# Performance work log

Measured on AMD Instinct MI355X. Metric: run time of the kernel, lower is better.

The kernel has to match this reference:

```python
import jax, jax.numpy as jnp
import numpy as np

D_MODEL = 1024
NUM_HEADS = 16
HEAD_DIM = D_MODEL // NUM_HEADS


def setup_inputs() -> dict:
    key = jax.random.key(0)
    ks = jax.random.split(key, 5)
    x = jax.random.normal(ks[0], (2, 2048, D_MODEL), dtype=jnp.float32)
    # torch nn.Linear init scale ~ U(-1/sqrt(in), 1/sqrt(in)); use small normals
    s = 1.0 / np.sqrt(D_MODEL)
    W_qkv = jax.random.normal(ks[1], (D_MODEL, 3 * D_MODEL), dtype=jnp.float32) * s
    b_qkv = jax.random.normal(ks[2], (3 * D_MODEL,), dtype=jnp.float32) * s
    W_out = jax.random.normal(ks[3], (D_MODEL, D_MODEL), dtype=jnp.float32) * s
    b_out = jax.random.normal(ks[4], (D_MODEL,), dtype=jnp.float32) * s
    return {"x": x, "W_qkv": W_qkv, "b_qkv": b_qkv, "W_out": W_out, "b_out": b_out}


def reference(x, W_qkv, b_qkv, W_out, b_out):
    B, S, _ = x.shape
    qkv = x @ W_qkv + b_qkv                                  # [B,S,3D]
    qkv = qkv.reshape(B, S, NUM_HEADS, 3 * HEAD_DIM).transpose(0, 2, 1, 3)  # [B,H,S,3d]
    q, k, v = jnp.split(qkv, 3, axis=-1)                     # each [B,H,S,d]
    scale = 1.0 / np.sqrt(HEAD_DIM)
    scores = jnp.einsum("bhqd,bhkd->bhqk", q, k) * scale      # [B,H,S,S]
    attn = jax.nn.softmax(scores, axis=-1)
    values = jnp.einsum("bhqk,bhkd->bhqd", attn, v)           # [B,H,S,d]
    values = values.transpose(0, 2, 1, 3).reshape(B, S, D_MODEL)
    return values @ W_out + b_out
```

## Files before the change

### kernel.cpp

```cpp
#include <hip/hip_runtime.h>


#define D_MODEL 1024
#define NHEAD   16
#define HDIM    64
#define SEQ     2048
#define BATCH   2
#define NTOK    (BATCH * SEQ)

typedef float    f32x4  __attribute__((ext_vector_type(4)));
typedef float    f32x16 __attribute__((ext_vector_type(16)));
typedef _Float16 f16x8  __attribute__((ext_vector_type(8)));
typedef _Float16 f16x4  __attribute__((ext_vector_type(4)));

#define GLOBAL_LOAD_LDS16(gptr, lptr)                                            \
    __builtin_amdgcn_global_load_lds(                                            \
        (const __attribute__((address_space(1))) unsigned int*)(gptr),           \
        (__attribute__((address_space(3))) unsigned int*)(lptr), 16, 0, 0)

__global__ __launch_bounds__(256) void prep_kernel(
    const float* __restrict__ x, _Float16* __restrict__ xh,
    const float* __restrict__ Wqkv, _Float16* __restrict__ wq_t,
    const float* __restrict__ Wout, _Float16* __restrict__ wo_t)
{
    const int bx = blockIdx.x;
    const int tid = threadIdx.x;
    if (bx < 4096) {
        const int i = (bx * 256 + tid) * 4;
        const float4 v = *(const float4*)&x[i];
        f16x4 hh;
        hh[0] = (_Float16)v.x; hh[1] = (_Float16)v.y;
        hh[2] = (_Float16)v.z; hh[3] = (_Float16)v.w;
        *(f16x4*)&xh[i] = hh;
        return;
    }
    __shared__ float ts[64][65];
    const float* W; _Float16* Wt; int N, n0, k0;
    if (bx < 4096 + 768) {
        const int local = bx - 4096;
        W = Wqkv; Wt = wq_t; N = 3072;
        n0 = (local % 48) * 64; k0 = (local / 48) * 64;
    } else {
        const int local = bx - 4864;
        W = Wout; Wt = wo_t; N = 1024;
        n0 = (local % 16) * 64; k0 = (local / 16) * 64;
    }
    {
        const int r = tid >> 2, c = (tid & 3) << 4;
        const float* src = W + (size_t)(k0 + r) * N + n0 + c;
        #pragma unroll
        for (int u = 0; u < 4; ++u)
            *(float4*)&ts[r][c + u * 4] = *(const float4*)&src[u * 4];
    }
    __syncthreads();
    {
        const int n = tid >> 2, kg = (tid & 3) << 4;
        f16x8 v0, v1;
        #pragma unroll
        for (int j = 0; j < 8; ++j) {
            v0[j] = (_Float16)ts[kg + j][n];
            v1[j] = (_Float16)ts[kg + 8 + j][n];
        }
        _Float16* dst = Wt + (size_t)(n0 + n) * D_MODEL + k0 + kg;
        *(f16x8*)&dst[0] = v0;
        *(f16x8*)&dst[8] = v1;
    }
}

__global__ __launch_bounds__(512) void gemm_qkv_kernel(
    const _Float16* __restrict__ A, const _Float16* __restrict__ Bt,
    const float* __restrict__ bias, _Float16* __restrict__ Qh,
    _Float16* __restrict__ Ksw, _Float16* __restrict__ Vsw,
    int M, int N, int K)
{
    __shared__ _Float16 lds[3][2][4096];
    const int tid = threadIdx.x;
    const int wave = tid >> 6, lane = tid & 63;
    const int quad = lane >> 4, l16 = lane & 15;
    const int m0 = blockIdx.y * 128, n0 = blockIdx.x * 128;
    const int wr = wave >> 1, wc = wave & 1;

    f32x4 acc[2][4] = {};

    const bool isA = wave < 4;
    const _Float16* gsrc = isA ? (A + (size_t)m0 * K) : (Bt + (size_t)n0 * K);
    const int plane = isA ? 0 : 1;
    const int sbase = (wave & 3) * 2;

#define G1_STAGE(tt, bi) {                                                     \
        const int _k1 = (tt) * 32;                                             \
        _Pragma("unroll")                                                      \
        for (int _j = 0; _j < 2; ++_j) {                                       \
            const int _seg = sbase + _j;                                       \
            const int _row = ((_seg & 1) << 6) | lane;                         \
            GLOBAL_LOAD_LDS16(gsrc + (size_t)_row * K + _k1 + (_seg >> 1) * 8, \
                              &lds[bi][plane][_seg * 512]);                    \
        } }

#define G1_COMPUTE(bi) {                                                       \
        f16x8 a[2], b[4];                                                      \
        _Pragma("unroll")                                                      \
        for (int mt = 0; mt < 2; ++mt)                                         \
            a[mt] = *(const f16x8*)&lds[bi][0][quad * 1024 + (wr * 32 + mt * 16 + l16) * 8]; \
        _Pragma("unroll")                                                      \
        for (int nt = 0; nt < 4; ++nt)                                         \
            b[nt] = *(const f16x8*)&lds[bi][1][quad * 1024 + (wc * 64 + nt * 16 + l16) * 8]; \
        __builtin_amdgcn_s_setprio(1);                                         \
        _Pragma("unroll")                                                      \
        for (int mt = 0; mt < 2; ++mt)                                         \
            _Pragma("unroll")                                                  \
            for (int nt = 0; nt < 4; ++nt)                                     \
                acc[mt][nt] = __builtin_amdgcn_mfma_f32_16x16x32_f16(a[mt], b[nt], acc[mt][nt], 0, 0, 0); \
        __builtin_amdgcn_s_setprio(0); }

#define G1_KSTEP(t, gatestr) {                                                 \
        const int _cur = (t) % 3;                                              \
        if ((t) + 2 < nk) { G1_STAGE((t) + 2, ((t) + 2) % 3); }                \
        asm volatile("s_waitcnt " gatestr ::: "memory");                       \
        __builtin_amdgcn_s_barrier();                                          \
        __builtin_amdgcn_sched_barrier(0);                                     \
        G1_COMPUTE(_cur);                                                      \
        __builtin_amdgcn_sched_barrier(0);                                     \
        __builtin_amdgcn_s_barrier();                                          \
        __builtin_amdgcn_sched_barrier(0);                                     \
    }

    const int nk = K / 32;
    G1_STAGE(0, 0);
    G1_STAGE(1, 1);

    for (int t = 0; t < nk - 2; ++t)
        G1_KSTEP(t, "vmcnt(4)");
    G1_KSTEP(nk - 2, "vmcnt(2)");
    G1_KSTEP(nk - 1, "vmcnt(0)");

#undef G1_KSTEP
#undef G1_COMPUTE
#undef G1_STAGE

    const int colb = n0 + wc * 64;
    const int kind = (colb >> 6) % 3;
    const int h    = colb / 192;
    const int bb   = m0 >> 11;
    const int m0r  = m0 & 2047;
    const size_t hsz = (size_t)8 * SEQ * 8;

    if (kind == 0) {
        _Float16* qh = Qh + (size_t)m0 * D_MODEL + h * HDIM;
        #pragma unroll
        for (int nt = 0; nt < 4; ++nt) {
            const float bv = bias[colb + nt * 16 + l16];
            #pragma unroll
            for (int mt = 0; mt < 2; ++mt) {
                #pragma unroll
                for (int r = 0; r < 4; ++r) {
                    const int row = wr * 32 + mt * 16 + quad * 4 + r;
                    qh[(size_t)row * D_MODEL + nt * 16 + l16] = (_Float16)(acc[mt][nt][r] + bv);
                }
            }
        }
    } else if (kind == 1) {
        _Float16* kh = Ksw + (size_t)(bb * NHEAD + h) * hsz;
        #pragma unroll
        for (int nt = 0; nt < 4; ++nt) {
            const int d = nt * 16 + l16;
            const float bv = bias[colb + nt * 16 + l16];
            _Float16* kd = kh + (size_t)(d >> 3) * (SEQ * 8) + (d & 7);
            #pragma unroll
            for (int mt = 0; mt < 2; ++mt) {
                #pragma unroll
                for (int r = 0; r < 4; ++r) {
                    const int s = m0r + wr * 32 + mt * 16 + quad * 4 + r;
                    kd[(size_t)s * 8] = (_Float16)(acc[mt][nt][r] + bv);
                }
            }
        }
    } else {
        _Float16* vh = Vsw + (size_t)(bb * NHEAD + h) * hsz;
        #pragma unroll
        for (int nt = 0; nt < 4; ++nt) {
            const int d = nt * 16 + l16;
            const float bv = bias[colb + nt * 16 + l16];
            #pragma unroll
            for (int mt = 0; mt < 2; ++mt) {
                const int s0 = m0r + wr * 32 + mt * 16 + quad * 4;
                f16x4 pk;
                #pragma unroll
                for (int r = 0; r < 4; ++r)
                    pk[r] = (_Float16)(acc[mt][nt][r] + bv);
                *(f16x4*)&vh[(size_t)(s0 >> 3) * 512 + d * 8 + (s0 & 7)] = pk;
            }
        }
    }
}

__global__ __launch_bounds__(512) void gemm_out_kernel(
    const _Float16* __restrict__ A, const _Float16* __restrict__ Bt,
    const float* __restrict__ bias, float* __restrict__ Cout)
{
    const int K = D_MODEL, N = D_MODEL;
    __shared__ _Float16 ldsA[2][4096];
    __shared__ _Float16 ldsB[2][2048];
    const int tid = threadIdx.x;
    const int wave = tid >> 6, lane = tid & 63;
    const int quad = lane >> 4, l16 = lane & 15;
    const int m0 = blockIdx.y * 128, n0 = blockIdx.x * 64;
    const int wr = wave >> 1, wc = wave & 1;

    f32x4 acc[2][2] = {};

    if (wave < 4) {
        #pragma unroll
        for (int j = 0; j < 2; ++j) {
            const int seg = wave * 2 + j;
            const int chunk = seg >> 1;
            const int row = ((seg & 1) << 6) | lane;
            GLOBAL_LOAD_LDS16(A + (size_t)(m0 + row) * K + chunk * 8, &ldsA[0][seg * 512]);
        }
    } else {
        const int seg = wave - 4;
        GLOBAL_LOAD_LDS16(Bt + (size_t)(n0 + lane) * K + seg * 8, &ldsB[0][seg * 512]);
    }
    __syncthreads();

    const int nk = K / 32;
    for (int t = 0; t < nk; ++t) {
        const int cur = t & 1;

        if (t + 1 < nk) {
            const int k1 = (t + 1) * 32;
            if (wave < 4) {
                #pragma unroll
                for (int j = 0; j < 2; ++j) {
                    const int seg = wave * 2 + j;
                    const int chunk = seg >> 1;
                    const int row = ((seg & 1) << 6) | lane;
                    GLOBAL_LOAD_LDS16(A + (size_t)(m0 + row) * K + k1 + chunk * 8,
                                      &ldsA[cur ^ 1][seg * 512]);
                }
            } else {
                const int seg = wave - 4;
                GLOBAL_LOAD_LDS16(Bt + (size_t)(n0 + lane) * K + k1 + seg * 8,
                                  &ldsB[cur ^ 1][seg * 512]);
            }
        }

        f16x8 a[2], b[2];
        #pragma unroll
        for (int mt = 0; mt < 2; ++mt)
            a[mt] = *(const f16x8*)&ldsA[cur][quad * 1024 + (wr * 32 + mt * 16 + l16) * 8];
        #pragma unroll
        for (int nt = 0; nt < 2; ++nt)
            b[nt] = *(const f16x8*)&ldsB[cur][quad * 512 + (wc * 32 + nt * 16 + l16) * 8];
        #pragma unroll
        for (int mt = 0; mt < 2; ++mt)
            #pragma unroll
            for (int nt = 0; nt < 2; ++nt)
                acc[mt][nt] = __builtin_amdgcn_mfma_f32_16x16x32_f16(a[mt], b[nt], acc[mt][nt], 0, 0, 0);

        __syncthreads();
    }

    #pragma unroll
    for (int nt = 0; nt < 2; ++nt) {
        const int col = n0 + wc * 32 + nt * 16 + l16;
        const float bv = bias[col];
        #pragma unroll
        for (int mt = 0; mt < 2; ++mt) {
            #pragma unroll
            for (int r = 0; r < 4; ++r) {
                const int row = m0 + wr * 32 + mt * 16 + quad * 4 + r;
                Cout[(size_t)row * N + col] = acc[mt][nt][r] + bv;
            }
        }
    }
}

__device__ __forceinline__ void softmax_frag(
    const f32x16 s0, const f32x16 s1, float& rs, f16x8 pa[4])
{
    #pragma unroll
    for (int half = 0; half < 2; ++half) {
        const f32x16 sv = half ? s1 : s0;
        float p[16];
        #pragma unroll
        for (int r = 0; r < 16; ++r)
            p[r] = __builtin_amdgcn_exp2f(sv[r]);
        #pragma unroll
        for (int r = 0; r < 16; r += 4)
            rs += (p[r] + p[r + 1]) + (p[r + 2] + p[r + 3]);

        union { f16x8 hv; unsigned u[4]; } lo, hh;
        {
            const unsigned A = __builtin_bit_cast(unsigned, __builtin_amdgcn_cvt_pkrtz(p[0], p[1]));
            const unsigned B = __builtin_bit_cast(unsigned, __builtin_amdgcn_cvt_pkrtz(p[2], p[3]));
            const unsigned C = __builtin_bit_cast(unsigned, __builtin_amdgcn_cvt_pkrtz(p[4], p[5]));
            const unsigned D = __builtin_bit_cast(unsigned, __builtin_amdgcn_cvt_pkrtz(p[6], p[7]));
            const auto rac = __builtin_amdgcn_permlane32_swap(A, C, false, false);
            const auto rbd = __builtin_amdgcn_permlane32_swap(B, D, false, false);
            lo.u[0] = rac[0]; lo.u[1] = rbd[0]; lo.u[2] = rac[1]; lo.u[3] = rbd[1];
        }
        {
            const unsigned E = __builtin_bit_cast(unsigned, __builtin_amdgcn_cvt_pkrtz(p[8],  p[9]));
            const unsigned F = __builtin_bit_cast(unsigned, __builtin_amdgcn_cvt_pkrtz(p[10], p[11]));
            const unsigned G = __builtin_bit_cast(unsigned, __builtin_amdgcn_cvt_pkrtz(p[12], p[13]));
            const unsigned H = __builtin_bit_cast(unsigned, __builtin_amdgcn_cvt_pkrtz(p[14], p[15]));
            const auto reg = __builtin_amdgcn_permlane32_swap(E, G, false, false);
            const auto rfh = __builtin_amdgcn_permlane32_swap(F, H, false, false);
            hh.u[0] = reg[0]; hh.u[1] = rfh[0]; hh.u[2] = reg[1]; hh.u[3] = rfh[1];
        }
        pa[half * 2]     = lo.hv;
        pa[half * 2 + 1] = hh.hv;
    }
}

__global__ __launch_bounds__(512) void attn_mfma_kernel(
    const _Float16* __restrict__ Qh,
    const _Float16* __restrict__ Ksw, const _Float16* __restrict__ Vsw,
    _Float16* __restrict__ val)
{
    __shared__ _Float16 Ks[2][8192];
    __shared__ _Float16 Vts[2][8192];

    const int tid = threadIdx.x;
    const int wave = tid >> 6, lane = tid & 63;
    const int l31 = lane & 31, hi = lane >> 5;

    const int id = blockIdx.x;
    const int g  = (id & 7) * 32 + (id >> 3);
    const int qt = g & 7, hb = g >> 3;
    const int h  = hb & 15, b = hb >> 4;
    const int q0 = qt * 256;

    const size_t hsz = (size_t)8 * SEQ * 8;
    const _Float16* kh = Ksw + (size_t)(b * NHEAD + h) * hsz;
    const _Float16* vh = Vsw + (size_t)(b * NHEAD + h) * hsz;

    f16x8 qf[4];
    {
        const int row = q0 + wave * 32 + l31;
        const _Float16* src = Qh + (size_t)(b * SEQ + row) * D_MODEL + h * HDIM + hi * 8;
        #pragma unroll
        for (int kk = 0; kk < 4; ++kk) {
            const f16x8 t = *(const f16x8*)(src + kk * 16);
            #pragma unroll
            for (int j = 0; j < 8; ++j)
                qf[kk][j] = (_Float16)((float)t[j] * 0.1803368802f);
        }
    }

    f32x16 acc0 = {};
    f32x16 acc1 = {};
    float rs = 0.f;

    const int sidx0 = wave * 2;
    #pragma unroll
    for (int j = 0; j < 2; ++j) {
        const int idx = sidx0 + j;
        const int u = idx >> 3, c = idx & 7;
        GLOBAL_LOAD_LDS16(kh + ((size_t)c * SEQ + u * 64 + lane) * 8, &Ks[0][idx * 512]);
        GLOBAL_LOAD_LDS16(vh + ((size_t)(u * 8 + c) * HDIM + lane) * 8, &Vts[0][idx * 512]);
    }
    __syncthreads();

    for (int kt = 0; kt < SEQ / 128; ++kt) {
        const int cur = kt & 1;

        if (kt + 1 < SEQ / 128) {
            #pragma unroll
            for (int j = 0; j < 2; ++j) {
                const int idx = sidx0 + j;
                const int u = idx >> 3, c = idx & 7;
                GLOBAL_LOAD_LDS16(kh + ((size_t)c * SEQ + (kt + 1) * 128 + u * 64 + lane) * 8,
                                  &Ks[cur ^ 1][idx * 512]);
                GLOBAL_LOAD_LDS16(vh + ((size_t)((kt + 1) * 16 + u * 8 + c) * HDIM + lane) * 8,
                                  &Vts[cur ^ 1][idx * 512]);
            }
        }

        #pragma unroll
        for (int u = 0; u < 2; ++u) {
            const _Float16* ksub = &Ks[cur][u * 4096];
            const _Float16* vsub = &Vts[cur][u * 4096];

            f32x16 s0 = {}, s1 = {};
            __builtin_amdgcn_s_setprio(1);
            #pragma unroll
            for (int kk = 0; kk < 4; ++kk) {
                const f16x8 k0 = *(const f16x8*)&ksub[(kk * 2 + hi) * 512 + l31 * 8];
                const f16x8 k1 = *(const f16x8*)&ksub[(kk * 2 + hi) * 512 + (32 + l31) * 8];
                s0 = __builtin_amdgcn_mfma_f32_32x32x16_f16(k0, qf[kk], s0, 0, 0, 0);
                s1 = __builtin_amdgcn_mfma_f32_32x32x16_f16(k1, qf[kk], s1, 0, 0, 0);
            }
            __builtin_amdgcn_s_setprio(0);

            f16x8 pa[4];
            softmax_frag(s0, s1, rs, pa);

            __builtin_amdgcn_s_setprio(1);
            #pragma unroll
            for (int ks = 0; ks < 4; ++ks) {
                const f16x8 v0 = *(const f16x8*)&vsub[(ks * 2 + hi) * 512 + l31 * 8];
                const f16x8 v1 = *(const f16x8*)&vsub[(ks * 2 + hi) * 512 + (32 + l31) * 8];
                acc0 = __builtin_amdgcn_mfma_f32_32x32x16_f16(pa[ks], v0, acc0, 0, 0, 0);
                acc1 = __builtin_amdgcn_mfma_f32_32x32x16_f16(pa[ks], v1, acc1, 0, 0, 0);
            }
            __builtin_amdgcn_s_setprio(0);
        }

        __syncthreads();
    }

    rs += __shfl_xor(rs, 32);
    const float inv = 1.f / rs;

    #pragma unroll
    for (int r = 0; r < 16; ++r) {
        const int qo = (r & 3) + 8 * (r >> 2) + 4 * hi;
        const float invr = __shfl(inv, qo);
        const int row = b * SEQ + q0 + wave * 32 + qo;
        val[(size_t)row * D_MODEL + h * HDIM + l31]      = (_Float16)(acc0[r] * invr);
        val[(size_t)row * D_MODEL + h * HDIM + 32 + l31] = (_Float16)(acc1[r] * invr);
    }
}

extern "C" void kernel_launch(void* const* d_in, const int* in_sizes, int n_in,
                              void* d_out, int out_size, void* d_ws, size_t ws_size,
                              hipStream_t stream)
{
    const float* x     = (const float*)d_in[0];
    const float* W_qkv = (const float*)d_in[1];
    const float* b_qkv = (const float*)d_in[2];
    const float* W_out = (const float*)d_in[3];
    const float* b_out = (const float*)d_in[4];

    char* ws = (char*)d_ws;
    _Float16* Ksw   = (_Float16*)ws;
    _Float16* val_h = (_Float16*)(ws + (8u << 20));
    _Float16* wq_t  = (_Float16*)(ws + (16u << 20));
    _Float16* wo_t  = (_Float16*)(ws + (22u << 20));
    _Float16* q_h   = (_Float16*)(ws + (24u << 20));
    _Float16* x_h   = (_Float16*)(ws + (32u << 20));
    _Float16* Vsw   = (_Float16*)(ws + (40u << 20));

    prep_kernel<<<5120, 256, 0, stream>>>(x, x_h, W_qkv, wq_t, W_out, wo_t);
    gemm_qkv_kernel<<<dim3(3 * D_MODEL / 128, NTOK / 128), 512, 0, stream>>>(
        x_h, wq_t, b_qkv, q_h, Ksw, Vsw, NTOK, 3 * D_MODEL, D_MODEL);
    attn_mfma_kernel<<<dim3(256, 1, 1), 512, 0, stream>>>(q_h, Ksw, Vsw, val_h);
    gemm_out_kernel<<<dim3(D_MODEL / 64, NTOK / 128), 512, 0, stream>>>(
        val_h, wo_t, b_out, (float*)d_out);
}
```

Measured before the change: 202.8 us.

## Triple-buffer out-projection GEMM loads with explicit vmcnt waits

Moves the output projection GEMM from a two-stage to a three-stage LDS ring, so global-to-LDS loads are issued two K-steps ahead. Per-wave `s_waitcnt vmcnt` thresholds replace the blanket `__syncthreads`, with raw barriers and scheduling fences around compute, and `setprio` is raised during the MFMAs. The aim is to hide global memory latency better in this GEMM. It costs extra LDS, which may reduce occupancy, and correctness now depends on hand-tuned wait counts.

```diff
diff --git a/kernel.cpp b/kernel.cpp
--- a/kernel.cpp
+++ b/kernel.cpp
@@ -199,8 +199,8 @@
     const float* __restrict__ bias, float* __restrict__ Cout)
 {
     const int K = D_MODEL, N = D_MODEL;
-    __shared__ _Float16 ldsA[2][4096];
-    __shared__ _Float16 ldsB[2][2048];
+    __shared__ _Float16 ldsA[3][4096];
+    __shared__ _Float16 ldsB[3][2048];
     const int tid = threadIdx.x;
     const int wave = tid >> 6, lane = tid & 63;
     const int quad = lane >> 4, l16 = lane & 15;
@@ -208,58 +208,65 @@
     const int wr = wave >> 1, wc = wave & 1;
 
     f32x4 acc[2][2] = {};
-
-    if (wave < 4) {
-        #pragma unroll
-        for (int j = 0; j < 2; ++j) {
-            const int seg = wave * 2 + j;
-            const int chunk = seg >> 1;
-            const int row = ((seg & 1) << 6) | lane;
-            GLOBAL_LOAD_LDS16(A + (size_t)(m0 + row) * K + chunk * 8, &ldsA[0][seg * 512]);
-        }
-    } else {
-        const int seg = wave - 4;
-        GLOBAL_LOAD_LDS16(Bt + (size_t)(n0 + lane) * K + seg * 8, &ldsB[0][seg * 512]);
-    }
-    __syncthreads();
+    const bool isA = wave < 4;
+
+#define G2_STAGE(tt, bi) {                                                     \
+        const int _k1 = (tt) * 32;                                             \
+        if (isA) {                                                             \
+            _Pragma("unroll")                                                  \
+            for (int _j = 0; _j < 2; ++_j) {                                   \
+                const int _seg = wave * 2 + _j;                                \
+                const int _row = ((_seg & 1) << 6) | lane;                     \
+                GLOBAL_LOAD_LDS16(A + (size_t)(m0 + _row) * K + _k1 + (_seg >> 1) * 8, \
+                                  &ldsA[bi][_seg * 512]);                      \
+            }                                                                  \
+        } else {                                                               \
+            const int _seg = wave - 4;                                         \
+            GLOBAL_LOAD_LDS16(Bt + (size_t)(n0 + lane) * K + _k1 + _seg * 8,   \
+                              &ldsB[bi][_seg * 512]);                          \
+        } }
+
+#define G2_COMPUTE(bi) {                                                       \
+        f16x8 a[2], b[2];                                                      \
+        _Pragma("unroll")                                                      \
+        for (int mt = 0; mt < 2; ++mt)                                         \
+            a[mt] = *(const f16x8*)&ldsA[bi][quad * 1024 + (wr * 32 + mt * 16 + l16) * 8]; \
+        _Pragma("unroll")                                                      \
+        for (int nt = 0; nt < 2; ++nt)                                         \
+            b[nt] = *(const f16x8*)&ldsB[bi][quad * 512 + (wc * 32 + nt * 16 + l16) * 8]; \
+        __builtin_amdgcn_s_setprio(1);                                         \
+        _Pragma("unroll")                                                      \
+        for (int mt = 0; mt < 2; ++mt)                                         \
+            _Pragma("unroll")                                                  \
+            for (int nt = 0; nt < 2; ++nt)                                     \
+                acc[mt][nt] = __builtin_amdgcn_mfma_f32_16x16x32_f16(a[mt], b[nt], acc[mt][nt], 0, 0, 0); \
+        __builtin_amdgcn_s_setprio(0); }
+
+#define G2_KSTEP(t, gA, gB) {                                                  \
+        const int _cur = (t) % 3;                                              \
+        if ((t) + 2 < nk) { G2_STAGE((t) + 2, ((t) + 2) % 3); }                \
+        if (isA) { asm volatile("s_waitcnt " gA ::: "memory"); }               \
+        else     { asm volatile("s_waitcnt " gB ::: "memory"); }               \
+        __builtin_amdgcn_s_barrier();                                          \
+        __builtin_amdgcn_sched_barrier(0);                                     \
+        G2_COMPUTE(_cur);                                                      \
+        __builtin_amdgcn_sched_barrier(0);                                     \
+        __builtin_amdgcn_s_barrier();                                          \
+        __builtin_amdgcn_sched_barrier(0);                                     \
+    }
 
     const int nk = K / 32;
-    for (int t = 0; t < nk; ++t) {
-        const int cur = t & 1;
-
-        if (t + 1 < nk) {
-            const int k1 = (t + 1) * 32;
-            if (wave < 4) {
-                #pragma unroll
-                for (int j = 0; j < 2; ++j) {
-                    const int seg = wave * 2 + j;
-                    const int chunk = seg >> 1;
-                    const int row = ((seg & 1) << 6) | lane;
-                    GLOBAL_LOAD_LDS16(A + (size_t)(m0 + row) * K + k1 + chunk * 8,
-                                      &ldsA[cur ^ 1][seg * 512]);
-                }
-            } else {
-                const int seg = wave - 4;
-                GLOBAL_LOAD_LDS16(Bt + (size_t)(n0 + lane) * K + k1 + seg * 8,
-                                  &ldsB[cur ^ 1][seg * 512]);
-            }
-        }
-
-        f16x8 a[2], b[2];
-        #pragma unroll
-        for (int mt = 0; mt < 2; ++mt)
-            a[mt] = *(const f16x8*)&ldsA[cur][quad * 1024 + (wr * 32 + mt * 16 + l16) * 8];
-        #pragma unroll
-        for (int nt = 0; nt < 2; ++nt)
-            b[nt] = *(const f16x8*)&ldsB[cur][quad * 512 + (wc * 32 + nt * 16 + l16) * 8];
-        #pragma unroll
-        for (int mt = 0; mt < 2; ++mt)
-            #pragma unroll
-            for (int nt = 0; nt < 2; ++nt)
-                acc[mt][nt] = __builtin_amdgcn_mfma_f32_16x16x32_f16(a[mt], b[nt], acc[mt][nt], 0, 0, 0);
-
-        __syncthreads();
-    }
+    G2_STAGE(0, 0);
+    G2_STAGE(1, 1);
+
+    for (int t = 0; t < nk - 2; ++t)
+        G2_KSTEP(t, "vmcnt(4)", "vmcnt(2)");
+    G2_KSTEP(nk - 2, "vmcnt(2)", "vmcnt(1)");
+    G2_KSTEP(nk - 1, "vmcnt(0)", "vmcnt(0)");
+
+#undef G2_KSTEP
+#undef G2_COMPUTE
+#undef G2_STAGE
 
     #pragma unroll
     for (int nt = 0; nt < 2; ++nt) {
```

New measurement: 206.1 us. No clear change (+1.6%).

## Drop LDS staging in attention; read K/V fragments directly from global

Applied to the files above, without the earlier changes.

The attention kernel no longer stages K and V tiles in double-buffered shared memory with async global-to-LDS loads and barriers. Each wave now loads its MFMA fragments straight from global memory (relying on L2/L1 for reuse across waves), iterating over 64-key chunks. Blocks shrink to 256 threads covering 128 queries, with twice as many blocks and a launch-bounds hint for 4 blocks per CU. This removes LDS traffic and block-wide syncs but multiplies global/cache reads of K/V by the number of waves sharing a head and exposes load latency without explicit prefetch.

```diff
diff --git a/kernel.cpp b/kernel.cpp
--- a/kernel.cpp
+++ b/kernel.cpp
@@ -314,23 +314,20 @@
     }
 }
 
-__global__ __launch_bounds__(512) void attn_mfma_kernel(
+__global__ __launch_bounds__(256, 4) void attn_mfma_kernel(
     const _Float16* __restrict__ Qh,
     const _Float16* __restrict__ Ksw, const _Float16* __restrict__ Vsw,
     _Float16* __restrict__ val)
 {
-    __shared__ _Float16 Ks[2][8192];
-    __shared__ _Float16 Vts[2][8192];
-
     const int tid = threadIdx.x;
     const int wave = tid >> 6, lane = tid & 63;
     const int l31 = lane & 31, hi = lane >> 5;
 
     const int id = blockIdx.x;
-    const int g  = (id & 7) * 32 + (id >> 3);
-    const int qt = g & 7, hb = g >> 3;
+    const int g  = (id & 7) * 64 + (id >> 3);
+    const int qt = g & 15, hb = g >> 4;
     const int h  = hb & 15, b = hb >> 4;
-    const int q0 = qt * 256;
+    const int q0 = qt * 128;
 
     const size_t hsz = (size_t)8 * SEQ * 8;
     const _Float16* kh = Ksw + (size_t)(b * NHEAD + h) * hsz;
@@ -353,62 +350,32 @@
     f32x16 acc1 = {};
     float rs = 0.f;
 
-    const int sidx0 = wave * 2;
-    #pragma unroll
-    for (int j = 0; j < 2; ++j) {
-        const int idx = sidx0 + j;
-        const int u = idx >> 3, c = idx & 7;
-        GLOBAL_LOAD_LDS16(kh + ((size_t)c * SEQ + u * 64 + lane) * 8, &Ks[0][idx * 512]);
-        GLOBAL_LOAD_LDS16(vh + ((size_t)(u * 8 + c) * HDIM + lane) * 8, &Vts[0][idx * 512]);
-    }
-    __syncthreads();
-
-    for (int kt = 0; kt < SEQ / 128; ++kt) {
-        const int cur = kt & 1;
-
-        if (kt + 1 < SEQ / 128) {
-            #pragma unroll
-            for (int j = 0; j < 2; ++j) {
-                const int idx = sidx0 + j;
-                const int u = idx >> 3, c = idx & 7;
-                GLOBAL_LOAD_LDS16(kh + ((size_t)c * SEQ + (kt + 1) * 128 + u * 64 + lane) * 8,
-                                  &Ks[cur ^ 1][idx * 512]);
-                GLOBAL_LOAD_LDS16(vh + ((size_t)((kt + 1) * 16 + u * 8 + c) * HDIM + lane) * 8,
-                                  &Vts[cur ^ 1][idx * 512]);
-            }
-        }
-
-        #pragma unroll
-        for (int u = 0; u < 2; ++u) {
-            const _Float16* ksub = &Ks[cur][u * 4096];
-            const _Float16* vsub = &Vts[cur][u * 4096];
-
-            f32x16 s0 = {}, s1 = {};
-            __builtin_amdgcn_s_setprio(1);
-            #pragma unroll
-            for (int kk = 0; kk < 4; ++kk) {
-                const f16x8 k0 = *(const f16x8*)&ksub[(kk * 2 + hi) * 512 + l31 * 8];
-                const f16x8 k1 = *(const f16x8*)&ksub[(kk * 2 + hi) * 512 + (32 + l31) * 8];
-                s0 = __builtin_amdgcn_mfma_f32_32x32x16_f16(k0, qf[kk], s0, 0, 0, 0);
-                s1 = __builtin_amdgcn_mfma_f32_32x32x16_f16(k1, qf[kk], s1, 0, 0, 0);
-            }
-            __builtin_amdgcn_s_setprio(0);
-
-            f16x8 pa[4];
-            softmax_frag(s0, s1, rs, pa);
-
-            __builtin_amdgcn_s_setprio(1);
-            #pragma unroll
-            for (int ks = 0; ks < 4; ++ks) {
-                const f16x8 v0 = *(const f16x8*)&vsub[(ks * 2 + hi) * 512 + l31 * 8];
-                const f16x8 v1 = *(const f16x8*)&vsub[(ks * 2 + hi) * 512 + (32 + l31) * 8];
-                acc0 = __builtin_amdgcn_mfma_f32_32x32x16_f16(pa[ks], v0, acc0, 0, 0, 0);
-                acc1 = __builtin_amdgcn_mfma_f32_32x32x16_f16(pa[ks], v1, acc1, 0, 0, 0);
-            }
-            __builtin_amdgcn_s_setprio(0);
-        }
-
-        __syncthreads();
+    for (int su = 0; su < SEQ / 64; ++su) {
+        f32x16 s0 = {}, s1 = {};
+        __builtin_amdgcn_s_setprio(1);
+        #pragma unroll
+        for (int kk = 0; kk < 4; ++kk) {
+            const _Float16* kc = kh + ((size_t)(kk * 2 + hi) * SEQ + su * 64) * 8;
+            const f16x8 k0 = *(const f16x8*)&kc[l31 * 8];
+            const f16x8 k1 = *(const f16x8*)&kc[(32 + l31) * 8];
+            s0 = __builtin_amdgcn_mfma_f32_32x32x16_f16(k0, qf[kk], s0, 0, 0, 0);
+            s1 = __builtin_amdgcn_mfma_f32_32x32x16_f16(k1, qf[kk], s1, 0, 0, 0);
+        }
+        __builtin_amdgcn_s_setprio(0);
+
+        f16x8 pa[4];
+        softmax_frag(s0, s1, rs, pa);
+
+        __builtin_amdgcn_s_setprio(1);
+        #pragma unroll
+        for (int ks = 0; ks < 4; ++ks) {
+            const _Float16* vc = vh + ((size_t)(su * 8 + ks * 2 + hi) * HDIM) * 8;
+            const f16x8 v0 = *(const f16x8*)&vc[l31 * 8];
+            const f16x8 v1 = *(const f16x8*)&vc[(32 + l31) * 8];
+            acc0 = __builtin_amdgcn_mfma_f32_32x32x16_f16(pa[ks], v0, acc0, 0, 0, 0);
+            acc1 = __builtin_amdgcn_mfma_f32_32x32x16_f16(pa[ks], v1, acc1, 0, 0, 0);
+        }
+        __builtin_amdgcn_s_setprio(0);
     }
 
     rs += __shfl_xor(rs, 32);
@@ -446,7 +413,7 @@
     prep_kernel<<<5120, 256, 0, stream>>>(x, x_h, W_qkv, wq_t, W_out, wo_t);
     gemm_qkv_kernel<<<dim3(3 * D_MODEL / 128, NTOK / 128), 512, 0, stream>>>(
         x_h, wq_t, b_qkv, q_h, Ksw, Vsw, NTOK, 3 * D_MODEL, D_MODEL);
-    attn_mfma_kernel<<<dim3(256, 1, 1), 512, 0, stream>>>(q_h, Ksw, Vsw, val_h);
+    attn_mfma_kernel<<<dim3(512, 1, 1), 256, 0, stream>>>(q_h, Ksw, Vsw, val_h);
     gemm_out_kernel<<<dim3(D_MODEL / 64, NTOK / 128), 512, 0, stream>>>(
         val_h, wo_t, b_out, (float*)d_out);
 }
```

Result: slower. 252.6 us (+24.5%).
